# Performance work log

Hardware: AMD Instinct MI355X
Metric: run time of the kernel (lower is better)

## Reference

```python
import jax, jax.numpy as jnp
import numpy as np

NUM_EMBEDDINGS = 512
EMBEDDING_DIM = 64


def setup_inputs() -> dict:
    key = jax.random.key(0)
    k_in, k_emb = jax.random.split(key)
    inputs = jax.random.normal(k_in, (8, 64, 16, 32, 32), dtype=jnp.float32)
    # matches torch uniform_(-1/K, 1/K) init
    lim = 1.0 / NUM_EMBEDDINGS
    embedding = jax.random.uniform(
        k_emb, (NUM_EMBEDDINGS, EMBEDDING_DIM), dtype=jnp.float32,
        minval=-lim, maxval=lim)
    return {"inputs": inputs, "embedding": embedding}


def reference(inputs, embedding):
    # inputs: (B, C=D, T, H, W); embedding: (K, D)
    x = jnp.transpose(inputs, (0, 2, 3, 4, 1))  # (B, T, H, W, D)
    in_shape = x.shape
    flat = x.reshape(-1, EMBEDDING_DIM)  # (N, D)
    distances = (
        jnp.sum(flat * flat, axis=1, keepdims=True)
        + jnp.sum(embedding * embedding, axis=1)
        - 2.0 * jnp.matmul(flat, embedding.T)
    )  # (N, K)
    # NOTE: original applies softmax to raw (positive) distances, faithfully kept
    weights = jax.nn.softmax(distances, axis=1)
    out = jnp.matmul(weights, embedding).reshape(in_shape)  # (B,T,H,W,D)
    return jnp.transpose(out, (0, 4, 1, 2, 3))  # (B, D, T, H, W)
```

## Files before the change

### kernel.cpp

```cpp
#include <hip/hip_runtime.h>
#include <hip/hip_bf16.h>

typedef __attribute__((ext_vector_type(8))) short short8;
typedef __attribute__((ext_vector_type(4))) short short4v;
typedef __attribute__((ext_vector_type(4))) _Float16 half4;
typedef __attribute__((ext_vector_type(4))) float f32x4;

#define SPW 16384
#define XST 72
#define RW  66
#define LOG2E 1.4426950408889634f

__device__ __forceinline__ float exp2_hw(float f) {
  return __builtin_amdgcn_exp2f(f);
}

__device__ __forceinline__ short bf16s(float f) {
  union { __hip_bfloat16 h; short s; } u;
  u.h = __float2bfloat16(f);
  return u.s;
}

__global__ void prep_all(const float* __restrict__ emb, short8* __restrict__ a1,
                         half4* __restrict__ eb, float* __restrict__ norms) {
  const int f = blockIdx.x * 256 + threadIdx.x;
  if (f < 4096) {
    const int l = f & 63;
    const int s = (f >> 6) & 1;
    const int m = f >> 7;
    const int row = m * 16 + (l & 15);
    const int col0 = s * 32 + (l >> 4) * 8;
    short8 v;
    #pragma unroll
    for (int i = 0; i < 8; ++i)
      v[i] = bf16s(-2.0f * LOG2E * emb[row * 64 + col0 + i]);
    a1[f] = v;
  } else if (f < 12288) {
    const int e = f - 4096;
    const int l = e & 63;
    const int m2 = (e >> 6) & 3;
    const int kt = e >> 8;
    const int d = m2 * 16 + (l & 15);
    const int k0 = kt * 16 + 4 * (l >> 4);
    half4 v;
    #pragma unroll
    for (int i = 0; i < 4; ++i) v[i] = (_Float16)emb[(k0 + i) * 64 + d];
    eb[e] = v;
  } else if (f < 12800) {
    const int k = f - 12288;
    float acc = 0.f;
    #pragma unroll
    for (int d = 0; d < 64; ++d) { float e = emb[k * 64 + d]; acc += e * e; }
    norms[k] = acc * LOG2E;
  }
}

__global__ __launch_bounds__(256, 4) void vq_main(
    const float* __restrict__ x, const short8* __restrict__ a1,
    const half4* __restrict__ eb, const float* __restrict__ norms,
    float* __restrict__ out) {
  __shared__ __align__(16) char lds_raw[17408];
  short* Xl   = reinterpret_cast<short*>(lds_raw);
  float* Rf   = reinterpret_cast<float*>(lds_raw);
  float* denl = reinterpret_cast<float*>(lds_raw + 16896);

  const int t = threadIdx.x;
  const int lane = t & 63;
  const int w = t >> 6;
  const int l15 = lane & 15;
  const int g = lane >> 4;

  const int tile = blockIdx.x * 32;
  const int b = tile >> 14;
  const int off = tile & 16383;
  const float* xb = x + (size_t)b * (64 * SPW) + off;
  float* ob = out + (size_t)b * (64 * SPW) + off;

  if (t < 128) {
    const int n0 = 4 * (t & 7);
    const int d0 = 4 * (t >> 3);
    const float4 r0 = *reinterpret_cast<const float4*>(xb + (size_t)(d0 + 0) * SPW + n0);
    const float4 r1 = *reinterpret_cast<const float4*>(xb + (size_t)(d0 + 1) * SPW + n0);
    const float4 r2 = *reinterpret_cast<const float4*>(xb + (size_t)(d0 + 2) * SPW + n0);
    const float4 r3 = *reinterpret_cast<const float4*>(xb + (size_t)(d0 + 3) * SPW + n0);
    const short4v c0 = {bf16s(r0.x), bf16s(r1.x), bf16s(r2.x), bf16s(r3.x)};
    const short4v c1 = {bf16s(r0.y), bf16s(r1.y), bf16s(r2.y), bf16s(r3.y)};
    const short4v c2 = {bf16s(r0.z), bf16s(r1.z), bf16s(r2.z), bf16s(r3.z)};
    const short4v c3 = {bf16s(r0.w), bf16s(r1.w), bf16s(r2.w), bf16s(r3.w)};
    *reinterpret_cast<short4v*>(&Xl[(n0 + 0) * XST + d0]) = c0;
    *reinterpret_cast<short4v*>(&Xl[(n0 + 1) * XST + d0]) = c1;
    *reinterpret_cast<short4v*>(&Xl[(n0 + 2) * XST + d0]) = c2;
    *reinterpret_cast<short4v*>(&Xl[(n0 + 3) * XST + d0]) = c3;
  }
  __syncthreads();

  short8 bx[2][2];
  #pragma unroll
  for (int j = 0; j < 2; ++j) {
    const int base = (j * 16 + l15) * XST + g * 8;
    bx[j][0] = *reinterpret_cast<const short8*>(&Xl[base]);
    bx[j][1] = *reinterpret_cast<const short8*>(&Xl[base + 32]);
  }

  f32x4 pacc[2][4];
  #pragma unroll
  for (int j = 0; j < 2; ++j)
    #pragma unroll
    for (int m2 = 0; m2 < 4; ++m2) pacc[j][m2] = f32x4{0.f, 0.f, 0.f, 0.f};
  float denp[2] = {0.f, 0.f};

  #pragma unroll 2
  for (int q = 0; q < 8; ++q) {
    const int kt = w * 8 + q;
    const short8 a1f0 = a1[(kt * 2 + 0) * 64 + lane];
    const short8 a1f1 = a1[(kt * 2 + 1) * 64 + lane];
    const half4 e0 = eb[(kt * 4 + 0) * 64 + lane];
    const half4 e1 = eb[(kt * 4 + 1) * 64 + lane];
    const half4 e2 = eb[(kt * 4 + 2) * 64 + lane];
    const half4 e3 = eb[(kt * 4 + 3) * 64 + lane];
    const float4 nv = *reinterpret_cast<const float4*>(&norms[kt * 16 + g * 4]);
    #pragma unroll
    for (int j = 0; j < 2; ++j) {
      f32x4 z = {0.f, 0.f, 0.f, 0.f};
      z = __builtin_amdgcn_mfma_f32_16x16x32_bf16(a1f0, bx[j][0], z, 0, 0, 0);
      z = __builtin_amdgcn_mfma_f32_16x16x32_bf16(a1f1, bx[j][1], z, 0, 0, 0);
      const float p0 = exp2_hw(nv.x + z[0]);
      const float p1 = exp2_hw(nv.y + z[1]);
      const float p2 = exp2_hw(nv.z + z[2]);
      const float p3 = exp2_hw(nv.w + z[3]);
      denp[j] += (p0 + p1) + (p2 + p3);
      const half4 pa = {(_Float16)p0, (_Float16)p1, (_Float16)p2, (_Float16)p3};
      pacc[j][0] = __builtin_amdgcn_mfma_f32_16x16x16f16(pa, e0, pacc[j][0], 0, 0, 0);
      pacc[j][1] = __builtin_amdgcn_mfma_f32_16x16x16f16(pa, e1, pacc[j][1], 0, 0, 0);
      pacc[j][2] = __builtin_amdgcn_mfma_f32_16x16x16f16(pa, e2, pacc[j][2], 0, 0, 0);
      pacc[j][3] = __builtin_amdgcn_mfma_f32_16x16x16f16(pa, e3, pacc[j][3], 0, 0, 0);
    }
  }

  #pragma unroll
  for (int j = 0; j < 2; ++j) {
    denp[j] += __shfl_xor(denp[j], 16, 64);
    denp[j] += __shfl_xor(denp[j], 32, 64);
  }
  if (lane < 16) {
    denl[w * 32 + l15] = denp[0];
    denl[w * 32 + 16 + l15] = denp[1];
  }

  const int n16 = t & 15;
  const int dq2 = t >> 4;
  #pragma unroll
  for (int j = 0; j < 2; ++j) {
    __syncthreads();
    #pragma unroll
    for (int m2 = 0; m2 < 4; ++m2)
      #pragma unroll
      for (int r = 0; r < 4; ++r)
        Rf[(w * 16 + 4 * g + r) * RW + m2 * 16 + l15] = pacc[j][m2][r];
    __syncthreads();
    const float den = (denl[j * 16 + n16] + denl[32 + j * 16 + n16])
                    + (denl[64 + j * 16 + n16] + denl[96 + j * 16 + n16]);
    const float rdv = 1.0f / den;
    #pragma unroll
    for (int r = 0; r < 4; ++r) {
      const int dd = r * 16 + dq2;
      const float sum = (Rf[n16 * RW + dd] + Rf[(16 + n16) * RW + dd])
                      + (Rf[(32 + n16) * RW + dd] + Rf[(48 + n16) * RW + dd]);
      ob[(size_t)dd * SPW + j * 16 + n16] = sum * rdv;
    }
  }
}

extern "C" void kernel_launch(void* const* d_in, const int* in_sizes, int n_in,
                              void* d_out, int out_size, void* d_ws, size_t ws_size,
                              hipStream_t stream) {
  (void)in_sizes; (void)n_in; (void)out_size; (void)ws_size;
  const float* x   = (const float*)d_in[0];
  const float* emb = (const float*)d_in[1];
  float* out = (float*)d_out;

  char* ws = (char*)d_ws;
  short8* a1   = (short8*)ws;
  half4*  eb   = (half4*)(ws + 65536);
  float*  norms = (float*)(ws + 131072);

  prep_all<<<50, 256, 0, stream>>>(emb, a1, eb, norms);
  vq_main<<<4096, 256, 0, stream>>>(x, a1, eb, norms, out);
}
```

Before: 45.43 us.

## Enlarge tile to 128 points per block with 2x2 wave split over points and codes

Each block now handles 128 spatial points instead of 32. Waves are split into two column groups and two codebook halves, so each wave reuses its loaded codebook fragments across four point sub-tiles. The cross-wave reduction is now a single LDS accumulate rather than a four-way sum, and output is written with float4 stores. The aim is fewer codebook fragment loads per point and wider global stores, at the cost of more registers, more LDS, a lower occupancy target of 3 waves and a quarter as many blocks.

```diff
diff --git a/kernel.cpp b/kernel.cpp
--- a/kernel.cpp
+++ b/kernel.cpp
@@ -8,7 +8,7 @@
 
 #define SPW 16384
 #define XST 72
-#define RW  66
+#define RW  67
 #define LOG2E 1.4426950408889634f
 
 __device__ __forceinline__ float exp2_hw(float f) {
@@ -55,63 +55,71 @@
   }
 }
 
-__global__ __launch_bounds__(256, 4) void vq_main(
+__global__ __launch_bounds__(256, 3) void vq_main(
     const float* __restrict__ x, const short8* __restrict__ a1,
     const half4* __restrict__ eb, const float* __restrict__ norms,
     float* __restrict__ out) {
-  __shared__ __align__(16) char lds_raw[17408];
+  __shared__ __align__(16) char lds_raw[35840];
   short* Xl   = reinterpret_cast<short*>(lds_raw);
   float* Rf   = reinterpret_cast<float*>(lds_raw);
-  float* denl = reinterpret_cast<float*>(lds_raw + 16896);
+  float* denl = reinterpret_cast<float*>(lds_raw + 34304);
+  float* rden = reinterpret_cast<float*>(lds_raw + 35328);
 
   const int t = threadIdx.x;
   const int lane = t & 63;
   const int w = t >> 6;
+  const int cg = w & 1;
+  const int kg = w >> 1;
   const int l15 = lane & 15;
   const int g = lane >> 4;
 
-  const int tile = blockIdx.x * 32;
+  const int tile = blockIdx.x * 128;
   const int b = tile >> 14;
   const int off = tile & 16383;
   const float* xb = x + (size_t)b * (64 * SPW) + off;
   float* ob = out + (size_t)b * (64 * SPW) + off;
 
-  if (t < 128) {
-    const int n0 = 4 * (t & 7);
-    const int d0 = 4 * (t >> 3);
-    const float4 r0 = *reinterpret_cast<const float4*>(xb + (size_t)(d0 + 0) * SPW + n0);
-    const float4 r1 = *reinterpret_cast<const float4*>(xb + (size_t)(d0 + 1) * SPW + n0);
-    const float4 r2 = *reinterpret_cast<const float4*>(xb + (size_t)(d0 + 2) * SPW + n0);
-    const float4 r3 = *reinterpret_cast<const float4*>(xb + (size_t)(d0 + 3) * SPW + n0);
-    const short4v c0 = {bf16s(r0.x), bf16s(r1.x), bf16s(r2.x), bf16s(r3.x)};
-    const short4v c1 = {bf16s(r0.y), bf16s(r1.y), bf16s(r2.y), bf16s(r3.y)};
-    const short4v c2 = {bf16s(r0.z), bf16s(r1.z), bf16s(r2.z), bf16s(r3.z)};
-    const short4v c3 = {bf16s(r0.w), bf16s(r1.w), bf16s(r2.w), bf16s(r3.w)};
-    *reinterpret_cast<short4v*>(&Xl[(n0 + 0) * XST + d0]) = c0;
-    *reinterpret_cast<short4v*>(&Xl[(n0 + 1) * XST + d0]) = c1;
-    *reinterpret_cast<short4v*>(&Xl[(n0 + 2) * XST + d0]) = c2;
-    *reinterpret_cast<short4v*>(&Xl[(n0 + 3) * XST + d0]) = c3;
+  {
+    const int n0 = 4 * (t & 15);
+    const int d0 = 4 * (t >> 4);
+    #pragma unroll
+    for (int h = 0; h < 2; ++h) {
+      const int nb = h * 64 + n0;
+      const float4 r0 = *reinterpret_cast<const float4*>(xb + (size_t)(d0 + 0) * SPW + nb);
+      const float4 r1 = *reinterpret_cast<const float4*>(xb + (size_t)(d0 + 1) * SPW + nb);
+      const float4 r2 = *reinterpret_cast<const float4*>(xb + (size_t)(d0 + 2) * SPW + nb);
+      const float4 r3 = *reinterpret_cast<const float4*>(xb + (size_t)(d0 + 3) * SPW + nb);
+      const short4v c0 = {bf16s(r0.x), bf16s(r1.x), bf16s(r2.x), bf16s(r3.x)};
+      const short4v c1 = {bf16s(r0.y), bf16s(r1.y), bf16s(r2.y), bf16s(r3.y)};
+      const short4v c2 = {bf16s(r0.z), bf16s(r1.z), bf16s(r2.z), bf16s(r3.z)};
+      const short4v c3 = {bf16s(r0.w), bf16s(r1.w), bf16s(r2.w), bf16s(r3.w)};
+      *reinterpret_cast<short4v*>(&Xl[(nb + 0) * XST + d0]) = c0;
+      *reinterpret_cast<short4v*>(&Xl[(nb + 1) * XST + d0]) = c1;
+      *reinterpret_cast<short4v*>(&Xl[(nb + 2) * XST + d0]) = c2;
+      *reinterpret_cast<short4v*>(&Xl[(nb + 3) * XST + d0]) = c3;
+    }
   }
   __syncthreads();
 
-  short8 bx[2][2];
-  #pragma unroll
-  for (int j = 0; j < 2; ++j) {
-    const int base = (j * 16 + l15) * XST + g * 8;
+  short8 bx[4][2];
+  #pragma unroll
+  for (int j = 0; j < 4; ++j) {
+    const int base = (cg * 64 + j * 16 + l15) * XST + g * 8;
     bx[j][0] = *reinterpret_cast<const short8*>(&Xl[base]);
     bx[j][1] = *reinterpret_cast<const short8*>(&Xl[base + 32]);
   }
 
-  f32x4 pacc[2][4];
-  #pragma unroll
-  for (int j = 0; j < 2; ++j)
+  f32x4 pacc[4][4];
+  #pragma unroll
+  for (int j = 0; j < 4; ++j)
     #pragma unroll
     for (int m2 = 0; m2 < 4; ++m2) pacc[j][m2] = f32x4{0.f, 0.f, 0.f, 0.f};
-  float denp[2] = {0.f, 0.f};
-
-  #pragma unroll 2
-  for (int q = 0; q < 8; ++q) {
-    const int kt = w * 8 + q;
+  float denp[4] = {0.f, 0.f, 0.f, 0.f};
+
+  const int kbase = kg * 16;
+  #pragma unroll
+  for (int q = 0; q < 16; ++q) {
+    const int kt = kbase + q;
     const short8 a1f0 = a1[(kt * 2 + 0) * 64 + lane];
     const short8 a1f1 = a1[(kt * 2 + 1) * 64 + lane];
     const half4 e0 = eb[(kt * 4 + 0) * 64 + lane];
@@ -120,7 +128,7 @@
     const half4 e3 = eb[(kt * 4 + 3) * 64 + lane];
     const float4 nv = *reinterpret_cast<const float4*>(&norms[kt * 16 + g * 4]);
     #pragma unroll
-    for (int j = 0; j < 2; ++j) {
+    for (int j = 0; j < 4; ++j) {
       f32x4 z = {0.f, 0.f, 0.f, 0.f};
       z = __builtin_amdgcn_mfma_f32_16x16x32_bf16(a1f0, bx[j][0], z, 0, 0, 0);
       z = __builtin_amdgcn_mfma_f32_16x16x32_bf16(a1f1, bx[j][1], z, 0, 0, 0);
@@ -138,36 +146,51 @@
   }
 
   #pragma unroll
-  for (int j = 0; j < 2; ++j) {
+  for (int j = 0; j < 4; ++j) {
     denp[j] += __shfl_xor(denp[j], 16, 64);
     denp[j] += __shfl_xor(denp[j], 32, 64);
   }
   if (lane < 16) {
-    denl[w * 32 + l15] = denp[0];
-    denl[w * 32 + 16 + l15] = denp[1];
-  }
-
-  const int n16 = t & 15;
-  const int dq2 = t >> 4;
-  #pragma unroll
-  for (int j = 0; j < 2; ++j) {
-    __syncthreads();
-    #pragma unroll
-    for (int m2 = 0; m2 < 4; ++m2)
+    #pragma unroll
+    for (int j = 0; j < 4; ++j)
+      denl[kg * 128 + cg * 64 + j * 16 + l15] = denp[j];
+  }
+
+  if (kg == 0) {
+    #pragma unroll
+    for (int j = 0; j < 4; ++j)
       #pragma unroll
-      for (int r = 0; r < 4; ++r)
-        Rf[(w * 16 + 4 * g + r) * RW + m2 * 16 + l15] = pacc[j][m2][r];
-    __syncthreads();
-    const float den = (denl[j * 16 + n16] + denl[32 + j * 16 + n16])
-                    + (denl[64 + j * 16 + n16] + denl[96 + j * 16 + n16]);
-    const float rdv = 1.0f / den;
-    #pragma unroll
-    for (int r = 0; r < 4; ++r) {
-      const int dd = r * 16 + dq2;
-      const float sum = (Rf[n16 * RW + dd] + Rf[(16 + n16) * RW + dd])
-                      + (Rf[(32 + n16) * RW + dd] + Rf[(48 + n16) * RW + dd]);
-      ob[(size_t)dd * SPW + j * 16 + n16] = sum * rdv;
-    }
+      for (int m2 = 0; m2 < 4; ++m2)
+        #pragma unroll
+        for (int r = 0; r < 4; ++r)
+          Rf[(cg * 64 + j * 16 + 4 * g + r) * RW + m2 * 16 + l15] = pacc[j][m2][r];
+  }
+  __syncthreads();
+
+  if (kg == 1) {
+    #pragma unroll
+    for (int j = 0; j < 4; ++j)
+      #pragma unroll
+      for (int m2 = 0; m2 < 4; ++m2)
+        #pragma unroll
+        for (int r = 0; r < 4; ++r)
+          Rf[(cg * 64 + j * 16 + 4 * g + r) * RW + m2 * 16 + l15] += pacc[j][m2][r];
+  } else {
+    rden[t & 127] = 1.0f / (denl[t & 127] + denl[128 + (t & 127)]);
+  }
+  __syncthreads();
+
+  const int nq = t & 31;
+  const int n = 4 * nq;
+  const int dh = t >> 5;
+  #pragma unroll
+  for (int it = 0; it < 8; ++it) {
+    const int d = it * 8 + dh;
+    const float4 o = {Rf[(n + 0) * RW + d] * rden[n + 0],
+                      Rf[(n + 1) * RW + d] * rden[n + 1],
+                      Rf[(n + 2) * RW + d] * rden[n + 2],
+                      Rf[(n + 3) * RW + d] * rden[n + 3]};
+    *reinterpret_cast<float4*>(&ob[(size_t)d * SPW + n]) = o;
   }
 }
 
@@ -185,5 +208,5 @@
   float*  norms = (float*)(ws + 131072);
 
   prep_all<<<50, 256, 0, stream>>>(emb, a1, eb, norms);
-  vq_main<<<4096, 256, 0, stream>>>(x, a1, eb, norms, out);
-}
+  vq_main<<<1024, 256, 0, stream>>>(x, a1, eb, norms, out);
+}
```

Result: faster. 40.68 us (-10.5%).

## Halve per-block tile to 16 points and interleave codebook fragments per lane

Applied to the files above, without the earlier changes.

Each block now processes 16 spatial points instead of 32, doubling the grid to 8192 blocks, and the epilogue runs a single reduction pass instead of two. The prepped codebook fragments are re-laid out so each lane's pieces are contiguous, allowing wider per-lane loads. The norm bias is folded into the MFMA accumulator init, and the reduction LDS row stride is padded to 68. The trade-off is that every codebook fragment load is now amortized over half as many points, doubling per-point codebook traffic and MFMA A-operand reuse loss, in exchange for more parallelism and fewer registers.

```diff
diff --git a/kernel.cpp b/kernel.cpp
--- a/kernel.cpp
+++ b/kernel.cpp
@@ -2,13 +2,12 @@
 #include <hip/hip_bf16.h>
 
 typedef __attribute__((ext_vector_type(8))) short short8;
-typedef __attribute__((ext_vector_type(4))) short short4v;
 typedef __attribute__((ext_vector_type(4))) _Float16 half4;
 typedef __attribute__((ext_vector_type(4))) float f32x4;
 
 #define SPW 16384
 #define XST 72
-#define RW  66
+#define RW  68
 #define LOG2E 1.4426950408889634f
 
 __device__ __forceinline__ float exp2_hw(float f) {
@@ -21,31 +20,31 @@
   return u.s;
 }
 
-__global__ void prep_all(const float* __restrict__ emb, short8* __restrict__ a1,
-                         half4* __restrict__ eb, float* __restrict__ norms) {
+__global__ void prep_all(const float* __restrict__ emb, short8* __restrict__ a1b,
+                         half4* __restrict__ eb2, float* __restrict__ norms) {
   const int f = blockIdx.x * 256 + threadIdx.x;
   if (f < 4096) {
-    const int l = f & 63;
-    const int s = (f >> 6) & 1;
-    const int m = f >> 7;
-    const int row = m * 16 + (l & 15);
-    const int col0 = s * 32 + (l >> 4) * 8;
+    const int s = f & 1;
+    const int lane = (f >> 1) & 63;
+    const int kt = f >> 7;
+    const int row = kt * 16 + (lane & 15);
+    const int col0 = s * 32 + (lane >> 4) * 8;
     short8 v;
     #pragma unroll
     for (int i = 0; i < 8; ++i)
       v[i] = bf16s(-2.0f * LOG2E * emb[row * 64 + col0 + i]);
-    a1[f] = v;
+    a1b[f] = v;
   } else if (f < 12288) {
     const int e = f - 4096;
-    const int l = e & 63;
-    const int m2 = (e >> 6) & 3;
+    const int m2 = e & 3;
+    const int lane = (e >> 2) & 63;
     const int kt = e >> 8;
-    const int d = m2 * 16 + (l & 15);
-    const int k0 = kt * 16 + 4 * (l >> 4);
+    const int d = m2 * 16 + (lane & 15);
+    const int k0 = kt * 16 + 4 * (lane >> 4);
     half4 v;
     #pragma unroll
     for (int i = 0; i < 4; ++i) v[i] = (_Float16)emb[(k0 + i) * 64 + d];
-    eb[e] = v;
+    eb2[e] = v;
   } else if (f < 12800) {
     const int k = f - 12288;
     float acc = 0.f;
@@ -56,13 +55,13 @@
 }
 
 __global__ __launch_bounds__(256, 4) void vq_main(
-    const float* __restrict__ x, const short8* __restrict__ a1,
-    const half4* __restrict__ eb, const float* __restrict__ norms,
+    const float* __restrict__ x, const short8* __restrict__ a1b,
+    const half4* __restrict__ eb2, const float* __restrict__ norms,
     float* __restrict__ out) {
-  __shared__ __align__(16) char lds_raw[17408];
+  __shared__ __align__(16) char lds_raw[17664];
   short* Xl   = reinterpret_cast<short*>(lds_raw);
   float* Rf   = reinterpret_cast<float*>(lds_raw);
-  float* denl = reinterpret_cast<float*>(lds_raw + 16896);
+  float* denl = reinterpret_cast<float*>(lds_raw + 17408);
 
   const int t = threadIdx.x;
   const int lane = t & 63;
@@ -70,104 +69,81 @@
   const int l15 = lane & 15;
   const int g = lane >> 4;
 
-  const int tile = blockIdx.x * 32;
+  const int tile = blockIdx.x * 16;
   const int b = tile >> 14;
   const int off = tile & 16383;
   const float* xb = x + (size_t)b * (64 * SPW) + off;
   float* ob = out + (size_t)b * (64 * SPW) + off;
 
-  if (t < 128) {
-    const int n0 = 4 * (t & 7);
-    const int d0 = 4 * (t >> 3);
-    const float4 r0 = *reinterpret_cast<const float4*>(xb + (size_t)(d0 + 0) * SPW + n0);
-    const float4 r1 = *reinterpret_cast<const float4*>(xb + (size_t)(d0 + 1) * SPW + n0);
-    const float4 r2 = *reinterpret_cast<const float4*>(xb + (size_t)(d0 + 2) * SPW + n0);
-    const float4 r3 = *reinterpret_cast<const float4*>(xb + (size_t)(d0 + 3) * SPW + n0);
-    const short4v c0 = {bf16s(r0.x), bf16s(r1.x), bf16s(r2.x), bf16s(r3.x)};
-    const short4v c1 = {bf16s(r0.y), bf16s(r1.y), bf16s(r2.y), bf16s(r3.y)};
-    const short4v c2 = {bf16s(r0.z), bf16s(r1.z), bf16s(r2.z), bf16s(r3.z)};
-    const short4v c3 = {bf16s(r0.w), bf16s(r1.w), bf16s(r2.w), bf16s(r3.w)};
-    *reinterpret_cast<short4v*>(&Xl[(n0 + 0) * XST + d0]) = c0;
-    *reinterpret_cast<short4v*>(&Xl[(n0 + 1) * XST + d0]) = c1;
-    *reinterpret_cast<short4v*>(&Xl[(n0 + 2) * XST + d0]) = c2;
-    *reinterpret_cast<short4v*>(&Xl[(n0 + 3) * XST + d0]) = c3;
+  {
+    const int d = t >> 2;
+    const int n0 = (t & 3) * 4;
+    const float4 v = *reinterpret_cast<const float4*>(xb + (size_t)d * SPW + n0);
+    Xl[(n0 + 0) * XST + d] = bf16s(v.x);
+    Xl[(n0 + 1) * XST + d] = bf16s(v.y);
+    Xl[(n0 + 2) * XST + d] = bf16s(v.z);
+    Xl[(n0 + 3) * XST + d] = bf16s(v.w);
   }
   __syncthreads();
 
-  short8 bx[2][2];
+  const short8 bx0 = *reinterpret_cast<const short8*>(&Xl[l15 * XST + g * 8]);
+  const short8 bx1 = *reinterpret_cast<const short8*>(&Xl[l15 * XST + 32 + g * 8]);
+  __syncthreads();
+
+  f32x4 pacc[4];
   #pragma unroll
-  for (int j = 0; j < 2; ++j) {
-    const int base = (j * 16 + l15) * XST + g * 8;
-    bx[j][0] = *reinterpret_cast<const short8*>(&Xl[base]);
-    bx[j][1] = *reinterpret_cast<const short8*>(&Xl[base + 32]);
+  for (int m2 = 0; m2 < 4; ++m2) pacc[m2] = f32x4{0.f, 0.f, 0.f, 0.f};
+  float denp = 0.f;
+
+  #pragma unroll
+  for (int q = 0; q < 8; ++q) {
+    const int kt = w * 8 + q;
+    const short8* ap = &a1b[(kt * 64 + lane) * 2];
+    const short8 a1f0 = ap[0];
+    const short8 a1f1 = ap[1];
+    const half4* ep = &eb2[(kt * 64 + lane) * 4];
+    const half4 e0 = ep[0];
+    const half4 e1 = ep[1];
+    const half4 e2 = ep[2];
+    const half4 e3 = ep[3];
+    const float4 nv = *reinterpret_cast<const float4*>(&norms[kt * 16 + g * 4]);
+
+    f32x4 z = {nv.x, nv.y, nv.z, nv.w};
+    z = __builtin_amdgcn_mfma_f32_16x16x32_bf16(a1f0, bx0, z, 0, 0, 0);
+    z = __builtin_amdgcn_mfma_f32_16x16x32_bf16(a1f1, bx1, z, 0, 0, 0);
+    const float p0 = exp2_hw(z[0]);
+    const float p1 = exp2_hw(z[1]);
+    const float p2 = exp2_hw(z[2]);
+    const float p3 = exp2_hw(z[3]);
+    denp += (p0 + p1) + (p2 + p3);
+    const half4 pa = {(_Float16)p0, (_Float16)p1, (_Float16)p2, (_Float16)p3};
+    pacc[0] = __builtin_amdgcn_mfma_f32_16x16x16f16(pa, e0, pacc[0], 0, 0, 0);
+    pacc[1] = __builtin_amdgcn_mfma_f32_16x16x16f16(pa, e1, pacc[1], 0, 0, 0);
+    pacc[2] = __builtin_amdgcn_mfma_f32_16x16x16f16(pa, e2, pacc[2], 0, 0, 0);
+    pacc[3] = __builtin_amdgcn_mfma_f32_16x16x16f16(pa, e3, pacc[3], 0, 0, 0);
   }
 
-  f32x4 pacc[2][4];
-  #pragma unroll
-  for (int j = 0; j < 2; ++j)
-    #pragma unroll
-    for (int m2 = 0; m2 < 4; ++m2) pacc[j][m2] = f32x4{0.f, 0.f, 0.f, 0.f};
-  float denp[2] = {0.f, 0.f};
-
-  #pragma unroll 2
-  for (int q = 0; q < 8; ++q) {
-    const int kt = w * 8 + q;
-    const short8 a1f0 = a1[(kt * 2 + 0) * 64 + lane];
-    const short8 a1f1 = a1[(kt * 2 + 1) * 64 + lane];
-    const half4 e0 = eb[(kt * 4 + 0) * 64 + lane];
-    const half4 e1 = eb[(kt * 4 + 1) * 64 + lane];
-    const half4 e2 = eb[(kt * 4 + 2) * 64 + lane];
-    const half4 e3 = eb[(kt * 4 + 3) * 64 + lane];
-    const float4 nv = *reinterpret_cast<const float4*>(&norms[kt * 16 + g * 4]);
-    #pragma unroll
-    for (int j = 0; j < 2; ++j) {
-      f32x4 z = {0.f, 0.f, 0.f, 0.f};
-      z = __builtin_amdgcn_mfma_f32_16x16x32_bf16(a1f0, bx[j][0], z, 0, 0, 0);
-      z = __builtin_amdgcn_mfma_f32_16x16x32_bf16(a1f1, bx[j][1], z, 0, 0, 0);
-      const float p0 = exp2_hw(nv.x + z[0]);
-      const float p1 = exp2_hw(nv.y + z[1]);
-      const float p2 = exp2_hw(nv.z + z[2]);
-      const float p3 = exp2_hw(nv.w + z[3]);
-      denp[j] += (p0 + p1) + (p2 + p3);
-      const half4 pa = {(_Float16)p0, (_Float16)p1, (_Float16)p2, (_Float16)p3};
-      pacc[j][0] = __builtin_amdgcn_mfma_f32_16x16x16f16(pa, e0, pacc[j][0], 0, 0, 0);
-      pacc[j][1] = __builtin_amdgcn_mfma_f32_16x16x16f16(pa, e1, pacc[j][1], 0, 0, 0);
-      pacc[j][2] = __builtin_amdgcn_mfma_f32_16x16x16f16(pa, e2, pacc[j][2], 0, 0, 0);
-      pacc[j][3] = __builtin_amdgcn_mfma_f32_16x16x16f16(pa, e3, pacc[j][3], 0, 0, 0);
-    }
-  }
+  denp += __shfl_xor(denp, 16, 64);
+  denp += __shfl_xor(denp, 32, 64);
+  if (lane < 16) denl[w * 16 + l15] = denp;
 
   #pragma unroll
-  for (int j = 0; j < 2; ++j) {
-    denp[j] += __shfl_xor(denp[j], 16, 64);
-    denp[j] += __shfl_xor(denp[j], 32, 64);
-  }
-  if (lane < 16) {
-    denl[w * 32 + l15] = denp[0];
-    denl[w * 32 + 16 + l15] = denp[1];
-  }
+  for (int m2 = 0; m2 < 4; ++m2)
+    #pragma unroll
+    for (int r = 0; r < 4; ++r)
+      Rf[(w * 16 + 4 * g + r) * RW + m2 * 16 + l15] = pacc[m2][r];
+  __syncthreads();
 
   const int n16 = t & 15;
-  const int dq2 = t >> 4;
+  const int dq = t >> 4;
+  const float den = (denl[n16] + denl[16 + n16]) + (denl[32 + n16] + denl[48 + n16]);
+  const float rdv = 1.0f / den;
   #pragma unroll
-  for (int j = 0; j < 2; ++j) {
-    __syncthreads();
-    #pragma unroll
-    for (int m2 = 0; m2 < 4; ++m2)
-      #pragma unroll
-      for (int r = 0; r < 4; ++r)
-        Rf[(w * 16 + 4 * g + r) * RW + m2 * 16 + l15] = pacc[j][m2][r];
-    __syncthreads();
-    const float den = (denl[j * 16 + n16] + denl[32 + j * 16 + n16])
-                    + (denl[64 + j * 16 + n16] + denl[96 + j * 16 + n16]);
-    const float rdv = 1.0f / den;
-    #pragma unroll
-    for (int r = 0; r < 4; ++r) {
-      const int dd = r * 16 + dq2;
-      const float sum = (Rf[n16 * RW + dd] + Rf[(16 + n16) * RW + dd])
-                      + (Rf[(32 + n16) * RW + dd] + Rf[(48 + n16) * RW + dd]);
-      ob[(size_t)dd * SPW + j * 16 + n16] = sum * rdv;
-    }
+  for (int r = 0; r < 4; ++r) {
+    const int d = r * 16 + dq;
+    const float s = (Rf[n16 * RW + d] + Rf[(16 + n16) * RW + d])
+                  + (Rf[(32 + n16) * RW + d] + Rf[(48 + n16) * RW + d]);
+    ob[(size_t)d * SPW + n16] = s * rdv;
   }
 }
 
@@ -180,10 +156,10 @@
   float* out = (float*)d_out;
 
   char* ws = (char*)d_ws;
-  short8* a1   = (short8*)ws;
-  half4*  eb   = (half4*)(ws + 65536);
+  short8* a1b  = (short8*)ws;
+  half4*  eb2  = (half4*)(ws + 65536);
   float*  norms = (float*)(ws + 131072);
 
-  prep_all<<<50, 256, 0, stream>>>(emb, a1, eb, norms);
-  vq_main<<<4096, 256, 0, stream>>>(x, a1, eb, norms, out);
+  prep_all<<<52, 256, 0, stream>>>(emb, a1b, eb2, norms);
+  vq_main<<<8192, 256, 0, stream>>>(x, a1b, eb2, norms, out);
 }
```

After: 57.03 us. +25.5%, slower.
